# Performance work log

Measured on AMD Instinct MI355X. Metric: run time of the kernel, lower is better.

The kernel has to match this reference:

```python
import jax, jax.numpy as jnp
import numpy as np

B, R, N, E, D, H = 4, 10, 64, 64, 300, 512  # batch, rounds, nodes, neighbours(=nodes), numberbatch_dim, lstm_hidden
SLOPE = 0.2  # LeakyReLU negative slope from config['slope']


def _xavier_uniform(key, shape, gain=1.414):
    fan_in, fan_out = shape[0], shape[1]
    lim = gain * np.sqrt(6.0 / (fan_in + fan_out))
    return jax.random.uniform(key, shape, jnp.float32, -lim, lim)


def setup_inputs() -> dict:
    key = jax.random.key(0)
    k0, k1, k2, k3, k4 = jax.random.split(key, 5)
    return {
        "adj_list": jax.random.normal(k0, (B, R, N, E, D), jnp.float32),
        "original_nodes": jax.random.normal(k1, (B, R, N, D), jnp.float32),
        "ques_embed": jax.random.normal(k2, (B, R, H), jnp.float32),
        "W": _xavier_uniform(k3, (D + H, H)),
        "a": _xavier_uniform(k4, (2 * H, 1)),
    }


def reference(adj_list, original_nodes, ques_embed, W, a):
    d_in = original_nodes.shape[-1]
    h = W.shape[-1]
    # Split W so that concat([x, q]) @ W == x @ Wn + q @ Wq (avoids the explicit
    # repeat + concat in the original torch code; same math).
    Wn, Wq = W[:d_in], W[d_in:]
    q_proj = jnp.einsum('brq,qh->brh', ques_embed, Wq)              # (B,R,H)
    w_original = jnp.einsum('brnd,dh->brnh', original_nodes, Wn) + q_proj[:, :, None, :]      # (B,R,N,H)
    Wh = jnp.einsum('brned,dh->brneh', adj_list, Wn) + q_proj[:, :, None, None, :]            # (B,R,N,E,H)
    a1, a2 = a[:h, 0], a[h:, 0]
    # e[b,r,n,e] = leakyrelu( (w_original @ a1)[b,r,n] + (Wh @ a2)[b,r,n,e] )
    scores = jnp.einsum('brnh,h->brn', w_original, a1)[..., None] + jnp.einsum('brneh,h->brne', Wh, a2)
    scores = jnp.where(scores > 0, scores, SLOPE * scores)
    # Faithful to original: softmax over dim=1 (the rounds axis). Dropout omitted (eval mode).
    attn = jax.nn.softmax(scores, axis=1)                            # (B,R,N,E)
    # h_prime[b,r,i,h] = sum_j attn[b,r,i,j] * w_original[b,r,j,h]  (requires E == N)
    h_prime = jnp.einsum('brij,brjh->brih', attn, w_original)
    return jax.nn.elu(h_prime)  # concat=True branch
```

## Files before the change

### kernel.cpp

```cpp
#include <hip/hip_runtime.h>
#include <math.h>

namespace {
constexpr int B = 4, R = 10, N = 64, E = 64, D = 300, H = 512;
constexpr int BR = B * R;
constexpr int NE = N * E;
constexpr int S = BR * NE;
constexpr float SLOPE = 0.2f;
constexpr int WO_BLOCKS = BR * 8;

constexpr int OFF_V1  = 0;
constexpr int OFF_V2  = OFF_V1 + 300;
constexpr int OFF_U1  = OFF_V2 + 300;
constexpr int OFF_U2  = OFF_U1 + H;
constexpr int OFF_QP  = OFF_U2 + H;
constexpr int OFF_QA1 = OFF_QP + BR * H;
constexpr int OFF_QA2 = OFF_QA1 + BR;
constexpr int OFF_S1  = OFF_QA2 + BR;
constexpr int OFF_SC  = OFF_S1 + BR * N;
constexpr int OFF_WO  = OFF_SC + S;
}

__device__ inline float waveReduce(float v) {
#pragma unroll
  for (int o = 32; o > 0; o >>= 1) v += __shfl_xor(v, o, 64);
  return v;
}

__device__ inline float dot4(float4 a, float4 b) {
  return a.x * b.x + a.y * b.y + a.z * b.z + a.w * b.w;
}

__global__ __launch_bounds__(64) void k_vecs(const float* __restrict__ W,
                                             const float* __restrict__ a,
                                             float* __restrict__ ws) {
  int row = blockIdx.x;
  int lane = threadIdx.x;
  const float4* rf  = reinterpret_cast<const float4*>(W + (size_t)row * H);
  const float4* a1f = reinterpret_cast<const float4*>(a);
  const float4* a2f = reinterpret_cast<const float4*>(a + H);
  float4 x0 = rf[lane], x1 = rf[64 + lane];
  float4 p0 = a1f[lane], p1 = a1f[64 + lane];
  float4 q0 = a2f[lane], q1 = a2f[64 + lane];
  float s1 = dot4(x0, p0) + dot4(x1, p1);
  float s2 = dot4(x0, q0) + dot4(x1, q1);
  s1 = waveReduce(s1);
  s2 = waveReduce(s2);
  if (lane == 0) {
    if (row < D) { ws[OFF_V1 + row] = s1; ws[OFF_V2 + row] = s2; }
    else         { ws[OFF_U1 + (row - D)] = s1; ws[OFF_U2 + (row - D)] = s2; }
  }
}

__global__ __launch_bounds__(512) void k_qproj_s1(const float* __restrict__ ques,
                                                  const float* __restrict__ W,
                                                  const float* __restrict__ orig,
                                                  float* __restrict__ ws) {
  int br = blockIdx.x, h = threadIdx.x;
  __shared__ float qs[H];
  __shared__ float red[16];
  __shared__ float qa1s;
  qs[h] = ques[(size_t)br * H + h];
  __syncthreads();
  float ac0 = 0.f, ac1 = 0.f, ac2 = 0.f, ac3 = 0.f;
#pragma unroll 4
  for (int q = 0; q < H; q += 4) {
    ac0 = fmaf(qs[q + 0], W[(size_t)(D + q + 0) * H + h], ac0);
    ac1 = fmaf(qs[q + 1], W[(size_t)(D + q + 1) * H + h], ac1);
    ac2 = fmaf(qs[q + 2], W[(size_t)(D + q + 2) * H + h], ac2);
    ac3 = fmaf(qs[q + 3], W[(size_t)(D + q + 3) * H + h], ac3);
  }
  float acc = (ac0 + ac1) + (ac2 + ac3);
  ws[OFF_QP + br * H + h] = acc;
  float p1 = qs[h] * ws[OFF_U1 + h];
  float p2 = qs[h] * ws[OFF_U2 + h];
  p1 = waveReduce(p1);
  p2 = waveReduce(p2);
  int lane = h & 63, wave = h >> 6;
  if (lane == 0) { red[wave] = p1; red[8 + wave] = p2; }
  __syncthreads();
  if (h == 0) {
    float t1 = 0.f, t2 = 0.f;
#pragma unroll
    for (int i = 0; i < 8; ++i) { t1 += red[i]; t2 += red[8 + i]; }
    ws[OFF_QA1 + br] = t1;
    ws[OFF_QA2 + br] = t2;
    qa1s = t1;
  }
  __syncthreads();
  float qa1 = qa1s;
  const float4* vf = reinterpret_cast<const float4*>(ws + OFF_V1);
  float4 va = vf[lane];
  float4 vb = (lane < 11) ? vf[64 + lane] : make_float4(0.f, 0.f, 0.f, 0.f);
  for (int n2 = wave * 8; n2 < wave * 8 + 8; n2 += 2) {
    const float4* rf0 = reinterpret_cast<const float4*>(orig + ((size_t)br * N + n2) * D);
    const float4* rf1 = reinterpret_cast<const float4*>(orig + ((size_t)br * N + n2 + 1) * D);
    float a0 = dot4(rf0[lane], va);
    float a1 = dot4(rf1[lane], va);
    if (lane < 11) {
      a0 += dot4(rf0[64 + lane], vb);
      a1 += dot4(rf1[64 + lane], vb);
    }
#pragma unroll
    for (int o = 32; o > 0; o >>= 1) {
      a0 += __shfl_xor(a0, o, 64);
      a1 += __shfl_xor(a1, o, 64);
    }
    if (lane == 0) {
      ws[OFF_S1 + br * N + n2]     = a0 + qa1;
      ws[OFF_S1 + br * N + n2 + 1] = a1 + qa1;
    }
  }
}

__global__ __launch_bounds__(256) void k_attn_wo(const float* __restrict__ adj,
                                                 const float* __restrict__ orig,
                                                 const float* __restrict__ W,
                                                 float* __restrict__ ws) {
  __shared__ __align__(16) float sA[64 * 60];
  __shared__ __align__(16) float sB[60 * 64];
  if (blockIdx.x < WO_BLOCKS) {
    int bi = blockIdx.x;
    int br = bi >> 3, h0 = (bi & 7) * 64;
    int t = threadIdx.x;
    const float4* sBf = reinterpret_cast<const float4*>(sB);
    int tn = t >> 4, th = t & 15;
    float acc[4][4] = {};
    for (int k0 = 0; k0 < D; k0 += 60) {
      __syncthreads();
      for (int idx = t; idx < 64 * 60; idx += 256) {
        int n = idx / 60, kk = idx % 60;
        sA[idx] = orig[((size_t)br * N + n) * D + k0 + kk];
      }
      for (int idx = t; idx < 60 * 64; idx += 256) {
        int kk = idx >> 6, hh = idx & 63;
        sB[idx] = W[(size_t)(k0 + kk) * H + h0 + hh];
      }
      __syncthreads();
#pragma unroll 4
      for (int kk = 0; kk < 60; ++kk) {
        float av[4];
#pragma unroll
        for (int i = 0; i < 4; ++i) av[i] = sA[(tn * 4 + i) * 60 + kk];
        float4 bv = sBf[kk * 16 + th];
#pragma unroll
        for (int i = 0; i < 4; ++i) {
          acc[i][0] = fmaf(av[i], bv.x, acc[i][0]);
          acc[i][1] = fmaf(av[i], bv.y, acc[i][1]);
          acc[i][2] = fmaf(av[i], bv.z, acc[i][2]);
          acc[i][3] = fmaf(av[i], bv.w, acc[i][3]);
        }
      }
    }
#pragma unroll
    for (int i = 0; i < 4; ++i) {
      int n = tn * 4 + i;
#pragma unroll
      for (int j = 0; j < 4; ++j) {
        int h = h0 + th * 4 + j;
        ws[OFF_WO + ((size_t)br * N + n) * H + h] = acc[i][j] + ws[OFF_QP + br * H + h];
      }
    }
    return;
  }
  int wid = (blockIdx.x - WO_BLOCKS) * 4 + (threadIdx.x >> 6);
  int lane = threadIdx.x & 63;
  int b = wid >> 12, ne = wid & 4095, n = ne >> 6;
  const float4* vf = reinterpret_cast<const float4*>(ws + OFF_V2);
  float4 va = vf[lane];
  float4 vb = (lane < 11) ? vf[64 + lane] : make_float4(0.f, 0.f, 0.f, 0.f);
  const float* base = adj + ((size_t)b * R * N * E + ne) * D;
  float4 x[R], y[R];
#pragma unroll
  for (int r = 0; r < R; ++r)
    x[r] = reinterpret_cast<const float4*>(base + (size_t)r * N * E * D)[lane];
  if (lane < 11) {
#pragma unroll
    for (int r = 0; r < R; ++r)
      y[r] = reinterpret_cast<const float4*>(base + (size_t)r * N * E * D)[64 + lane];
  }
  int brb = b * R;
  float add[R];
#pragma unroll
  for (int r = 0; r < R; ++r)
    add[r] = ws[OFF_QA2 + brb + r] + ws[OFF_S1 + (brb + r) * N + n];
  float acc[R];
#pragma unroll
  for (int r = 0; r < R; ++r) acc[r] = dot4(x[r], va);
  if (lane < 11) {
#pragma unroll
    for (int r = 0; r < R; ++r) acc[r] += dot4(y[r], vb);
  }
#pragma unroll
  for (int o = 32; o > 0; o >>= 1) {
#pragma unroll
    for (int r = 0; r < R; ++r) acc[r] += __shfl_xor(acc[r], o, 64);
  }
  float m = -1e30f;
#pragma unroll
  for (int r = 0; r < R; ++r) {
    float sc = acc[r] + add[r];
    sc = sc > 0.f ? sc : SLOPE * sc;
    acc[r] = sc;
    m = fmaxf(m, sc);
  }
  float s = 0.f;
#pragma unroll
  for (int r = 0; r < R; ++r) { acc[r] = __expf(acc[r] - m); s += acc[r]; }
  float inv = 1.f / s;
  if (lane == 0) {
#pragma unroll
    for (int r = 0; r < R; ++r)
      ws[OFF_SC + (size_t)(brb + r) * NE + ne] = acc[r] * inv;
  }
}

__global__ __launch_bounds__(256) void k_hprime(const float* __restrict__ ws,
                                                float* __restrict__ out) {
  int br = blockIdx.x;
  int h = blockIdx.y * 64 + (threadIdx.x & 63);
  int ig = threadIdx.x >> 6;
  __shared__ __align__(16) float sAtt[64 * 64];
  const float* att = ws + OFF_SC + (size_t)br * NE;
  for (int idx = threadIdx.x; idx < 4096; idx += 256) sAtt[idx] = att[idx];
  __syncthreads();
  float acc[16] = {};
  const float* wo = ws + OFF_WO + (size_t)br * N * H;
  const float4* sAttf = reinterpret_cast<const float4*>(sAtt);
#pragma unroll 2
  for (int j4 = 0; j4 < 16; ++j4) {
    float w0 = wo[(size_t)(4 * j4 + 0) * H + h];
    float w1 = wo[(size_t)(4 * j4 + 1) * H + h];
    float w2 = wo[(size_t)(4 * j4 + 2) * H + h];
    float w3 = wo[(size_t)(4 * j4 + 3) * H + h];
#pragma unroll
    for (int ii = 0; ii < 16; ++ii) {
      float4 a4 = sAttf[(ig * 16 + ii) * 16 + j4];
      acc[ii] = fmaf(a4.x, w0, fmaf(a4.y, w1, fmaf(a4.z, w2, fmaf(a4.w, w3, acc[ii]))));
    }
  }
#pragma unroll
  for (int ii = 0; ii < 16; ++ii) {
    int i = ig * 16 + ii;
    float x = acc[ii];
    out[((size_t)br * N + i) * H + h] = x > 0.f ? x : expm1f(x);
  }
}

extern "C" void kernel_launch(void* const* d_in, const int* in_sizes, int n_in,
                              void* d_out, int out_size, void* d_ws, size_t ws_size,
                              hipStream_t stream) {
  const float* adj  = (const float*)d_in[0];
  const float* orig = (const float*)d_in[1];
  const float* ques = (const float*)d_in[2];
  const float* W    = (const float*)d_in[3];
  const float* a    = (const float*)d_in[4];
  float* out = (float*)d_out;
  float* ws  = (float*)d_ws;

  k_vecs<<<dim3(D + H), dim3(64), 0, stream>>>(W, a, ws);
  k_qproj_s1<<<dim3(BR), dim3(512), 0, stream>>>(ques, W, orig, ws);
  k_attn_wo<<<dim3(WO_BLOCKS + B * NE / 4), dim3(256), 0, stream>>>(adj, orig, W, ws);
  k_hprime<<<dim3(BR, 8), dim3(256), 0, stream>>>(ws, out);
}
```

Measured before the change: 113.8 us.

## Make attention waves persistent with double-buffered register prefetch of adj rows

The attention part of k_attn_wo now launches 1024 blocks instead of 4096, and each wave loops over four (b,n,e) units strided by the total wave count. The main float4 slice of the next unit's adj rows is loaded into a second register buffer while the current unit is reduced and softmaxed. The goal is to keep more global loads in flight per wave and cut block launch overhead on this memory-bound stream of adj data. The cost is higher register pressure from two R-sized float4 buffers, which may lower occupancy.

After: 104.8 us (median of 2 runs). -7.9%, faster.

```diff
diff --git a/kernel.cpp b/kernel.cpp
--- a/kernel.cpp
+++ b/kernel.cpp
@@ -8,6 +8,9 @@
 constexpr int S = BR * NE;
 constexpr float SLOPE = 0.2f;
 constexpr int WO_BLOCKS = BR * 8;
+constexpr int ATTN_BLOCKS = 1024;
+constexpr int ATTN_WAVES = ATTN_BLOCKS * 4;
+constexpr int UPW = (B * NE) / ATTN_WAVES;
 
 constexpr int OFF_V1  = 0;
 constexpr int OFF_V2  = OFF_V1 + 300;
@@ -113,6 +116,62 @@
   }
 }
 
+__device__ __forceinline__ void attn_load_x(const float* __restrict__ adj, int u,
+                                            int lane, float4 (&x)[R]) {
+  const float* base = adj + ((size_t)(u >> 12) * R * NE + (u & 4095)) * D;
+#pragma unroll
+  for (int r = 0; r < R; ++r)
+    x[r] = reinterpret_cast<const float4*>(base + (size_t)r * NE * D)[lane];
+}
+
+__device__ __forceinline__ void attn_compute(const float* __restrict__ adj,
+                                             float* __restrict__ ws, int u, int lane,
+                                             const float4 (&x)[R],
+                                             float4 va, float4 vb) {
+  int b = u >> 12, ne = u & 4095, n = ne >> 6, brb = b * R;
+  const float* base = adj + ((size_t)b * R * NE + ne) * D;
+  bool tl = lane < 11;
+  float4 y[R];
+  if (tl) {
+#pragma unroll
+    for (int r = 0; r < R; ++r)
+      y[r] = reinterpret_cast<const float4*>(base + (size_t)r * NE * D)[64 + lane];
+  }
+  float add[R];
+#pragma unroll
+  for (int r = 0; r < R; ++r)
+    add[r] = ws[OFF_QA2 + brb + r] + ws[OFF_S1 + (brb + r) * N + n];
+  float acc[R];
+#pragma unroll
+  for (int r = 0; r < R; ++r) acc[r] = dot4(x[r], va);
+  if (tl) {
+#pragma unroll
+    for (int r = 0; r < R; ++r) acc[r] += dot4(y[r], vb);
+  }
+#pragma unroll
+  for (int o = 32; o > 0; o >>= 1) {
+#pragma unroll
+    for (int r = 0; r < R; ++r) acc[r] += __shfl_xor(acc[r], o, 64);
+  }
+  float m = -1e30f;
+#pragma unroll
+  for (int r = 0; r < R; ++r) {
+    float sc = acc[r] + add[r];
+    sc = sc > 0.f ? sc : SLOPE * sc;
+    acc[r] = sc;
+    m = fmaxf(m, sc);
+  }
+  float s = 0.f;
+#pragma unroll
+  for (int r = 0; r < R; ++r) { acc[r] = __expf(acc[r] - m); s += acc[r]; }
+  float inv = 1.f / s;
+  if (lane == 0) {
+#pragma unroll
+    for (int r = 0; r < R; ++r)
+      ws[OFF_SC + (size_t)(brb + r) * NE + ne] = acc[r] * inv;
+  }
+}
+
 __global__ __launch_bounds__(256) void k_attn_wo(const float* __restrict__ adj,
                                                  const float* __restrict__ orig,
                                                  const float* __restrict__ W,
@@ -163,55 +222,22 @@
     }
     return;
   }
-  int wid = (blockIdx.x - WO_BLOCKS) * 4 + (threadIdx.x >> 6);
+  int aw = (blockIdx.x - WO_BLOCKS) * 4 + (threadIdx.x >> 6);
   int lane = threadIdx.x & 63;
-  int b = wid >> 12, ne = wid & 4095, n = ne >> 6;
   const float4* vf = reinterpret_cast<const float4*>(ws + OFF_V2);
   float4 va = vf[lane];
   float4 vb = (lane < 11) ? vf[64 + lane] : make_float4(0.f, 0.f, 0.f, 0.f);
-  const float* base = adj + ((size_t)b * R * N * E + ne) * D;
-  float4 x[R], y[R];
-#pragma unroll
-  for (int r = 0; r < R; ++r)
-    x[r] = reinterpret_cast<const float4*>(base + (size_t)r * N * E * D)[lane];
-  if (lane < 11) {
-#pragma unroll
-    for (int r = 0; r < R; ++r)
-      y[r] = reinterpret_cast<const float4*>(base + (size_t)r * N * E * D)[64 + lane];
-  }
-  int brb = b * R;
-  float add[R];
-#pragma unroll
-  for (int r = 0; r < R; ++r)
-    add[r] = ws[OFF_QA2 + brb + r] + ws[OFF_S1 + (brb + r) * N + n];
-  float acc[R];
-#pragma unroll
-  for (int r = 0; r < R; ++r) acc[r] = dot4(x[r], va);
-  if (lane < 11) {
-#pragma unroll
-    for (int r = 0; r < R; ++r) acc[r] += dot4(y[r], vb);
-  }
-#pragma unroll
-  for (int o = 32; o > 0; o >>= 1) {
-#pragma unroll
-    for (int r = 0; r < R; ++r) acc[r] += __shfl_xor(acc[r], o, 64);
-  }
-  float m = -1e30f;
-#pragma unroll
-  for (int r = 0; r < R; ++r) {
-    float sc = acc[r] + add[r];
-    sc = sc > 0.f ? sc : SLOPE * sc;
-    acc[r] = sc;
-    m = fmaxf(m, sc);
-  }
-  float s = 0.f;
-#pragma unroll
-  for (int r = 0; r < R; ++r) { acc[r] = __expf(acc[r] - m); s += acc[r]; }
-  float inv = 1.f / s;
-  if (lane == 0) {
-#pragma unroll
-    for (int r = 0; r < R; ++r)
-      ws[OFF_SC + (size_t)(brb + r) * NE + ne] = acc[r] * inv;
+  float4 xA[R], xB[R];
+  attn_load_x(adj, aw, lane, xA);
+#pragma unroll
+  for (int i = 0; i < UPW; ++i) {
+    int u = aw + i * ATTN_WAVES;
+    if (i + 1 < UPW) {
+      if (i & 1) attn_load_x(adj, aw + (i + 1) * ATTN_WAVES, lane, xA);
+      else       attn_load_x(adj, aw + (i + 1) * ATTN_WAVES, lane, xB);
+    }
+    if (i & 1) attn_compute(adj, ws, u, lane, xB, va, vb);
+    else       attn_compute(adj, ws, u, lane, xA, va, vb);
   }
 }
 
@@ -260,6 +286,6 @@
 
   k_vecs<<<dim3(D + H), dim3(64), 0, stream>>>(W, a, ws);
   k_qproj_s1<<<dim3(BR), dim3(512), 0, stream>>>(ques, W, orig, ws);
-  k_attn_wo<<<dim3(WO_BLOCKS + B * NE / 4), dim3(256), 0, stream>>>(adj, orig, W, ws);
+  k_attn_wo<<<dim3(WO_BLOCKS + ATTN_BLOCKS), dim3(256), 0, stream>>>(adj, orig, W, ws);
   k_hprime<<<dim3(BR, 8), dim3(256), 0, stream>>>(ws, out);
 }
```

## Split adj dot-products across 4-thread groups and move softmax into hprime kernel

Applied to the files above, without the earlier changes.

The adjacency-score pass now assigns each 300-float row to 4 threads instead of a full wave per (b,n,e) handling all 10 rounds. Each block writes raw dot products to the workspace, and the softmax over rounds moves into k_hprime, which recomputes it per (br, y-block). The W-projection tile shrinks from K=60 to K=30 to cut shared memory and allow more resident blocks. The cost is redundant softmax recomputation, 8 times per br across the y-blocks, plus reads of all 10 rounds' raw scores in k_hprime.

Result: slower. 122.1 us (+7.3%).

```diff
diff --git a/kernel.cpp b/kernel.cpp
--- a/kernel.cpp
+++ b/kernel.cpp
@@ -8,6 +8,7 @@
 constexpr int S = BR * NE;
 constexpr float SLOPE = 0.2f;
 constexpr int WO_BLOCKS = BR * 8;
+constexpr int S2_BLOCKS = S / 64;
 
 constexpr int OFF_V1  = 0;
 constexpr int OFF_V2  = OFF_V1 + 300;
@@ -17,8 +18,8 @@
 constexpr int OFF_QA1 = OFF_QP + BR * H;
 constexpr int OFF_QA2 = OFF_QA1 + BR;
 constexpr int OFF_S1  = OFF_QA2 + BR;
-constexpr int OFF_SC  = OFF_S1 + BR * N;
-constexpr int OFF_WO  = OFF_SC + S;
+constexpr int OFF_RAW = OFF_S1 + BR * N;
+constexpr int OFF_WO  = OFF_RAW + S;
 }
 
 __device__ inline float waveReduce(float v) {
@@ -113,35 +114,36 @@
   }
 }
 
-__global__ __launch_bounds__(256) void k_attn_wo(const float* __restrict__ adj,
-                                                 const float* __restrict__ orig,
-                                                 const float* __restrict__ W,
-                                                 float* __restrict__ ws) {
-  __shared__ __align__(16) float sA[64 * 60];
-  __shared__ __align__(16) float sB[60 * 64];
+__global__ __launch_bounds__(256) void k_s2_wo(const float* __restrict__ adj,
+                                               const float* __restrict__ orig,
+                                               const float* __restrict__ W,
+                                               float* __restrict__ ws) {
+  __shared__ __align__(16) float smem[64 * 30 + 30 * 64];
+  int t = threadIdx.x;
   if (blockIdx.x < WO_BLOCKS) {
     int bi = blockIdx.x;
     int br = bi >> 3, h0 = (bi & 7) * 64;
-    int t = threadIdx.x;
+    float* sA = smem;
+    float* sB = smem + 1920;
     const float4* sBf = reinterpret_cast<const float4*>(sB);
     int tn = t >> 4, th = t & 15;
     float acc[4][4] = {};
-    for (int k0 = 0; k0 < D; k0 += 60) {
+    for (int k0 = 0; k0 < D; k0 += 30) {
       __syncthreads();
-      for (int idx = t; idx < 64 * 60; idx += 256) {
-        int n = idx / 60, kk = idx % 60;
+      for (int idx = t; idx < 64 * 30; idx += 256) {
+        int n = idx / 30, kk = idx % 30;
         sA[idx] = orig[((size_t)br * N + n) * D + k0 + kk];
       }
-      for (int idx = t; idx < 60 * 64; idx += 256) {
+      for (int idx = t; idx < 30 * 64; idx += 256) {
         int kk = idx >> 6, hh = idx & 63;
         sB[idx] = W[(size_t)(k0 + kk) * H + h0 + hh];
       }
       __syncthreads();
-#pragma unroll 4
-      for (int kk = 0; kk < 60; ++kk) {
+#pragma unroll 5
+      for (int kk = 0; kk < 30; ++kk) {
         float av[4];
 #pragma unroll
-        for (int i = 0; i < 4; ++i) av[i] = sA[(tn * 4 + i) * 60 + kk];
+        for (int i = 0; i < 4; ++i) av[i] = sA[(tn * 4 + i) * 30 + kk];
         float4 bv = sBf[kk * 16 + th];
 #pragma unroll
         for (int i = 0; i < 4; ++i) {
@@ -163,67 +165,56 @@
     }
     return;
   }
-  int wid = (blockIdx.x - WO_BLOCKS) * 4 + (threadIdx.x >> 6);
-  int lane = threadIdx.x & 63;
-  int b = wid >> 12, ne = wid & 4095, n = ne >> 6;
-  const float4* vf = reinterpret_cast<const float4*>(ws + OFF_V2);
-  float4 va = vf[lane];
-  float4 vb = (lane < 11) ? vf[64 + lane] : make_float4(0.f, 0.f, 0.f, 0.f);
-  const float* base = adj + ((size_t)b * R * N * E + ne) * D;
-  float4 x[R], y[R];
-#pragma unroll
-  for (int r = 0; r < R; ++r)
-    x[r] = reinterpret_cast<const float4*>(base + (size_t)r * N * E * D)[lane];
-  if (lane < 11) {
-#pragma unroll
-    for (int r = 0; r < R; ++r)
-      y[r] = reinterpret_cast<const float4*>(base + (size_t)r * N * E * D)[64 + lane];
-  }
-  int brb = b * R;
-  float add[R];
-#pragma unroll
-  for (int r = 0; r < R; ++r)
-    add[r] = ws[OFF_QA2 + brb + r] + ws[OFF_S1 + (brb + r) * N + n];
-  float acc[R];
-#pragma unroll
-  for (int r = 0; r < R; ++r) acc[r] = dot4(x[r], va);
-  if (lane < 11) {
-#pragma unroll
-    for (int r = 0; r < R; ++r) acc[r] += dot4(y[r], vb);
-  }
-#pragma unroll
-  for (int o = 32; o > 0; o >>= 1) {
-#pragma unroll
-    for (int r = 0; r < R; ++r) acc[r] += __shfl_xor(acc[r], o, 64);
-  }
-  float m = -1e30f;
-#pragma unroll
-  for (int r = 0; r < R; ++r) {
-    float sc = acc[r] + add[r];
-    sc = sc > 0.f ? sc : SLOPE * sc;
-    acc[r] = sc;
-    m = fmaxf(m, sc);
-  }
-  float s = 0.f;
-#pragma unroll
-  for (int r = 0; r < R; ++r) { acc[r] = __expf(acc[r] - m); s += acc[r]; }
-  float inv = 1.f / s;
-  if (lane == 0) {
-#pragma unroll
-    for (int r = 0; r < R; ++r)
-      ws[OFF_SC + (size_t)(brb + r) * NE + ne] = acc[r] * inv;
-  }
+  for (int i = t; i < 300; i += 256) smem[i] = ws[OFF_V2 + i];
+  __syncthreads();
+  const float4* v4 = reinterpret_cast<const float4*>(smem);
+  int grp = t & 3;
+  int row = (blockIdx.x - WO_BLOCKS) * 64 + (t >> 2);
+  const float4* ap = reinterpret_cast<const float4*>(adj) + (size_t)row * 75;
+  float ac0 = 0.f, ac1 = 0.f;
+#pragma unroll
+  for (int j = 0; j < 19; ++j) {
+    int idx = grp + 4 * j;
+    if (j < 18 || grp < 3) {
+      float4 x = ap[idx];
+      float4 v = v4[idx];
+      if (j & 1) ac1 = fmaf(x.x, v.x, fmaf(x.y, v.y, fmaf(x.z, v.z, fmaf(x.w, v.w, ac1))));
+      else       ac0 = fmaf(x.x, v.x, fmaf(x.y, v.y, fmaf(x.z, v.z, fmaf(x.w, v.w, ac0))));
+    }
+  }
+  float acc = ac0 + ac1;
+  acc += __shfl_xor(acc, 1, 64);
+  acc += __shfl_xor(acc, 2, 64);
+  if (grp == 0) ws[OFF_RAW + row] = acc;
 }
 
 __global__ __launch_bounds__(256) void k_hprime(const float* __restrict__ ws,
                                                 float* __restrict__ out) {
   int br = blockIdx.x;
-  int h = blockIdx.y * 64 + (threadIdx.x & 63);
-  int ig = threadIdx.x >> 6;
+  int b = br / R, r = br % R;
+  int t = threadIdx.x;
   __shared__ __align__(16) float sAtt[64 * 64];
-  const float* att = ws + OFF_SC + (size_t)br * NE;
-  for (int idx = threadIdx.x; idx < 4096; idx += 256) sAtt[idx] = att[idx];
-  __syncthreads();
+  const float* raw = ws + OFF_RAW;
+  for (int ne = t; ne < NE; ne += 256) {
+    int n = ne >> 6;
+    float v[R];
+    float m = -1e30f;
+#pragma unroll
+    for (int rr = 0; rr < R; ++rr) {
+      int brr = b * R + rr;
+      float sc = raw[(size_t)brr * NE + ne] + ws[OFF_QA2 + brr] + ws[OFF_S1 + brr * N + n];
+      sc = sc > 0.f ? sc : SLOPE * sc;
+      v[rr] = sc;
+      m = fmaxf(m, sc);
+    }
+    float s = 0.f;
+#pragma unroll
+    for (int rr = 0; rr < R; ++rr) { v[rr] = __expf(v[rr] - m); s += v[rr]; }
+    sAtt[ne] = v[r] / s;
+  }
+  __syncthreads();
+  int h = blockIdx.y * 64 + (t & 63);
+  int ig = t >> 6;
   float acc[16] = {};
   const float* wo = ws + OFF_WO + (size_t)br * N * H;
   const float4* sAttf = reinterpret_cast<const float4*>(sAtt);
@@ -260,6 +251,6 @@
 
   k_vecs<<<dim3(D + H), dim3(64), 0, stream>>>(W, a, ws);
   k_qproj_s1<<<dim3(BR), dim3(512), 0, stream>>>(ques, W, orig, ws);
-  k_attn_wo<<<dim3(WO_BLOCKS + B * NE / 4), dim3(256), 0, stream>>>(adj, orig, W, ws);
+  k_s2_wo<<<dim3(WO_BLOCKS + S2_BLOCKS), dim3(256), 0, stream>>>(adj, orig, W, ws);
   k_hprime<<<dim3(BR, 8), dim3(256), 0, stream>>>(ws, out);
 }
```
